# Kernel optimization log

Hardware: AMD Instinct MI355X
Metric: run time of the kernel (lower is better)

## Reference

```python
import jax, jax.numpy as jnp
import numpy as np

TOP_K = 2  # config.moe_config['moe_top_k']


def setup_inputs() -> dict:
    key = jax.random.key(0)
    k1, k2, k3, k4 = jax.random.split(key, 4)
    B, S, H, F, E = 2, 1024, 1024, 2048, 8
    def init(k, shape, fan_in):
        return jax.random.normal(k, shape, jnp.float32) / np.float32(np.sqrt(fan_in))
    return {
        "hidden_states": jax.random.normal(k1, (B, S, H), jnp.float32),
        "router_w": init(k2, (H, E), H),          # Linear(hidden, E, bias=False)
        "W1": init(k3, (E, H, 2 * F), H),          # per-expert Linear(hidden, 2*ffn)
        "W2": init(k4, (E, F, H), F),              # per-expert Linear(ffn, hidden)
    }


def reference(hidden_states, router_w, W1, W2):
    B, S, H = hidden_states.shape
    E = router_w.shape[1]
    x = hidden_states.reshape(-1, H)                      # [N, H], N = B*S
    N = x.shape[0]

    # router: logits -> fp32 softmax -> top-k -> renormalize (matches torch)
    logits = x @ router_w                                  # [N, E]
    probs = jax.nn.softmax(logits.astype(jnp.float32), axis=-1)
    rw, sel = jax.lax.top_k(probs, TOP_K)                  # [N, k]
    rw = rw / rw.sum(axis=-1, keepdims=True)
    rw = rw.astype(x.dtype)

    # combine weights per (token, expert); top-k experts are distinct so add==set
    cw = jnp.zeros((N, E), x.dtype).at[jnp.arange(N)[:, None], sel].add(rw)

    # per-expert SwiGLU MLP over all tokens, masked combine (full-capacity MoE)
    h = jnp.einsum('nh,ehf->enf', x, W1)                   # [E, N, 2F]
    a, b = jnp.split(h, 2, axis=-1)                        # gate, value halves
    g = jax.nn.silu(a) * b                                 # [E, N, F]
    y = jnp.einsum('enf,efh->enh', g, W2)                  # [E, N, H]
    out = jnp.einsum('enh,ne->nh', y, cw)                  # weighted scatter-combine
    return out.reshape(B, S, H)
```

## Files before the change

kernel.cpp:

```cpp
#include <hip/hip_runtime.h>
#include <hip/hip_bf16.h>

#define H_DIM 1024
#define E_NUM 8
#define F_DIM 2048
#define N_TOK 2048
typedef unsigned int uint;
typedef short bf16x8 __attribute__((ext_vector_type(8)));
typedef float f32x4 __attribute__((ext_vector_type(4)));

#define WS_CNT   0
#define WS_OFF   64
#define WS_LIST  256
#define WS_W     (WS_LIST + 8*N_TOK*4)
#define WS_G     131072
#define WS_AX    (WS_G + 4096*2048*2)
#define WS_Y     WS_AX


static __device__ __forceinline__ uint f2bf(float f) {
    uint u = __builtin_bit_cast(uint, f);
    return (u + 0x7FFFu + ((u >> 16) & 1u)) >> 16;
}
static __device__ __forceinline__ float bflo(uint u) { return __builtin_bit_cast(float, u << 16); }
static __device__ __forceinline__ float bfhi(uint u) { return __builtin_bit_cast(float, u & 0xFFFF0000u); }
static __device__ __forceinline__ uint cvtpk(float a, float b) {
    uint r;
    asm("v_cvt_pk_bf16_f32 %0, %1, %2" : "=v"(r) : "v"(a), "v"(b));
    return r;
}
static __device__ __forceinline__ void gload_lds16(const void* g, void* l) {
    __builtin_amdgcn_global_load_lds(
        (const __attribute__((address_space(1))) unsigned int*)g,
        (__attribute__((address_space(3))) unsigned int*)l,
        16, 0, 0);
}
template<int N> static __device__ __forceinline__ void vmwait() {
    if constexpr (N == 0)      asm volatile("s_waitcnt vmcnt(0)" ::: "memory");
    else if constexpr (N == 2) asm volatile("s_waitcnt vmcnt(2)" ::: "memory");
    else if constexpr (N == 4) asm volatile("s_waitcnt vmcnt(4)" ::: "memory");
}
static __device__ __forceinline__ void lgk0_bar() {
    asm volatile("s_waitcnt lgkmcnt(0)" ::: "memory");
    __builtin_amdgcn_sched_barrier(0);
    __builtin_amdgcn_s_barrier();
    asm volatile("" ::: "memory");
}

__global__ __launch_bounds__(256) void router_kernel(
    const float* __restrict__ x, const float* __restrict__ rw,
    int* __restrict__ cnt, int* __restrict__ list, float* __restrict__ w_entry)
{
    int wave = threadIdx.x >> 6, lane = threadIdx.x & 63;
    int n = blockIdx.x * 4 + wave;
    const float* xr = x + (size_t)n * H_DIM;
    float acc[8] = {0,0,0,0,0,0,0,0};
    #pragma unroll
    for (int i = 0; i < H_DIM/64; ++i) {
        int h = i*64 + lane;
        float xv = xr[h];
        const float4* rr = (const float4*)(rw + (size_t)h*8);
        float4 r0 = rr[0], r1 = rr[1];
        acc[0] += xv*r0.x; acc[1] += xv*r0.y; acc[2] += xv*r0.z; acc[3] += xv*r0.w;
        acc[4] += xv*r1.x; acc[5] += xv*r1.y; acc[6] += xv*r1.z; acc[7] += xv*r1.w;
    }
    #pragma unroll
    for (int e = 0; e < 8; ++e) {
        float v = acc[e];
        #pragma unroll
        for (int off = 32; off; off >>= 1) v += __shfl_xor(v, off);
        acc[e] = v;
    }
    int e0 = 0;
    #pragma unroll
    for (int e = 1; e < 8; ++e) if (acc[e] > acc[e0]) e0 = e;
    int e1 = -1;
    #pragma unroll
    for (int e = 0; e < 8; ++e) if (e != e0 && (e1 < 0 || acc[e] > acc[e1])) e1 = e;
    float w0 = 1.0f / (1.0f + __expf(acc[e1] - acc[e0]));
    float w1 = 1.0f - w0;
    if (lane == 0) {
        int p0 = atomicAdd(&cnt[e0], 1);
        list[e0*N_TOK + p0] = n*2;
        w_entry[n*2] = w0;
        int p1 = atomicAdd(&cnt[e1], 1);
        list[e1*N_TOK + p1] = n*2 + 1;
        w_entry[n*2+1] = w1;
    }
}

__global__ void prefix_kernel(const int* __restrict__ cnt, int* __restrict__ off) {
    if (threadIdx.x == 0) {
        int s = 0;
        #pragma unroll
        for (int e = 0; e < E_NUM; ++e) { off[e] = s; s += cnt[e]; }
        off[E_NUM] = s;
    }
}

__global__ __launch_bounds__(256) void gather_kernel(
    const float* __restrict__ x, const int* __restrict__ cnt, const int* __restrict__ off,
    const int* __restrict__ list, unsigned short* __restrict__ Ax)
{
    int e = blockIdx.x >> 9;
    int r = (blockIdx.x & 511)*4 + (threadIdx.x >> 6);
    int lane = threadIdx.x & 63;
    if (r >= cnt[e]) return;
    int ent = list[e*N_TOK + r];
    const float* xr = x + (size_t)(ent >> 1) * H_DIM;
    unsigned short* dr = Ax + (size_t)(off[e] + r) * H_DIM;
    #pragma unroll
    for (int q = 0; q < 2; ++q) {
        int b = lane*2 + q;
        int t = b >> 3, s = b & 7;
        int klo = t*64 + (s >> 2)*32 + (s & 3)*4;
        float4 lo = *(const float4*)(xr + klo);
        float4 hi = *(const float4*)(xr + klo + 16);
        uint4 o;
        o.x = cvtpk(lo.x, lo.y); o.y = cvtpk(lo.z, lo.w);
        o.z = cvtpk(hi.x, hi.y); o.w = cvtpk(hi.z, hi.w);
        *(uint4*)(dr + b*8) = o;
    }
}

template<int IS_G1>
__global__ __launch_bounds__(256, IS_G1 ? 3 : 5) void moe_gemm_kernel(
    const unsigned short* __restrict__ Asrc, const float* __restrict__ W,
    const int* __restrict__ cnt, const int* __restrict__ off,
    const int* __restrict__ list, const float* __restrict__ w_entry,
    unsigned short* __restrict__ dst)
{
    constexpr int KTOT  = IS_G1 ? H_DIM : F_DIM;
    constexpr int BLD   = IS_G1 ? 2*F_DIM : H_DIM;
    constexpr int DLD   = IS_G1 ? F_DIM : H_DIM;
    constexpr int ALD   = IS_G1 ? H_DIM : F_DIM;
    constexpr int ROWS  = IS_G1 ? 128 : 64;
    constexpr int NM    = IS_G1 ? 8 : 2;
    constexpr int NA    = IS_G1 ? 4 : 2;
    constexpr int NMT   = IS_G1 ? 16 : 32;
    constexpr int NNT   = IS_G1 ? 32 : 16;
    constexpr int BSROW = IS_G1 ? 512 : 256;
    constexpr int NBS   = IS_G1 ? 2 : 1;
    constexpr int NT2   = KTOT / 64;

    __shared__ __align__(16) unsigned short As[2][ROWS*64];
    __shared__ __align__(16) uint Bs[2][16*BSROW/4];

    constexpr int nb = NMT * NNT * E_NUM;
    constexpr int chunk = nb >> 3;
    int bid = blockIdx.x;
    int f  = (bid & 7) * chunk + (bid >> 3);
    int mt = f % NMT;
    int nt = (f / NMT) % NNT;
    int e  = f / (NMT * NNT);

    const int c = cnt[e];
    if (mt * ROWS >= c) return;
    const int abase = off[e] + mt * ROWS;
    const int tid = threadIdx.x;
    const int lane = tid & 63, wid = tid >> 6;
    const int l15 = lane & 15, lg = lane >> 4;
    const int wr = IS_G1 ? 0 : (wid >> 1);
    const int wc = wid & 1;
    const int rowbase = IS_G1 ? 0 : wr*32;

    const unsigned short* a_src[NA];
    #pragma unroll
    for (int i = 0; i < NA; ++i) {
        int sl  = wid*(NA*1024) + i*1024 + lane*16;
        int row = sl >> 7;
        int kb  = ((sl >> 4) & 7) ^ (row & 7);
        int gr  = abase + row; gr = gr < 4095 ? gr : 4095;
        a_src[i] = Asrc + (size_t)gr * ALD + kb*8;
    }

    const float* Wb = W + (size_t)e * (size_t)(IS_G1 ? H_DIM*2*F_DIM : F_DIM*H_DIM);
    const float* b_src[NBS]; int b_dst[NBS];
    #pragma unroll
    for (int s = 0; s < NBS; ++s) {
        int q = tid + s*256;
        int kp, c4, gc;
        if constexpr (IS_G1) {
            kp = q >> 5; c4 = q & 31;
            gc = (c4 < 16) ? (nt*64 + 4*c4) : (F_DIM + nt*64 + 4*(c4-16));
        } else {
            kp = q >> 4; c4 = q & 15;
            gc = nt*64 + 4*c4;
        }
        b_src[s] = Wb + (size_t)(2*kp) * BLD + gc;
        b_dst[s] = (kp*BSROW + c4*16) ^ ((kp & 4) << 4);
    }

    int a_addr[NM][2];
    #pragma unroll
    for (int m = 0; m < NM; ++m)
        #pragma unroll
        for (int p = 0; p < 2; ++p) {
            int row = rowbase + m*16 + l15;
            a_addr[m][p] = row*128 + ((p*64 + lg*16) ^ ((row & 7) << 4));
        }
    int b_base[2];
    const int xorv = ((2*lg) & 4) << 4;
    #pragma unroll
    for (int j = 0; j < 2; ++j) {
        int cb = IS_G1 ? (j ? (4 + wid) : wid) : (wc*2 + j);
        b_base[j] = (2*lg)*BSROW + (((cb*16 + l15) * 4) ^ xorv);
    }

    f32x4 acc[NM][2];
    #pragma unroll
    for (int m = 0; m < NM; ++m)
        #pragma unroll
        for (int j = 0; j < 2; ++j) acc[m][j] = (f32x4){0.f,0.f,0.f,0.f};

    struct BQ { float4 r0[NBS], r1[NBS]; };
    auto loadB = [&](int t) {
        BQ q;
        #pragma unroll
        for (int s = 0; s < NBS; ++s) {
            const float* p = b_src[s] + (size_t)t * 32 * BLD;
            q.r0[s] = *(const float4*)p;
            q.r1[s] = *(const float4*)(p + BLD);
        }
        return q;
    };
    auto dswB = [&](const BQ& q, int buf) {
        #pragma unroll
        for (int s = 0; s < NBS; ++s) {
            uint4 w4;
            w4.x = cvtpk(q.r0[s].x, q.r1[s].x); w4.y = cvtpk(q.r0[s].y, q.r1[s].y);
            w4.z = cvtpk(q.r0[s].z, q.r1[s].z); w4.w = cvtpk(q.r0[s].w, q.r1[s].w);
            *(uint4*)((char*)Bs[buf] + b_dst[s]) = w4;
        }
    };
    auto STAGE_A = [&](int a) {
        #pragma unroll
        for (int i = 0; i < NA; ++i)
            gload_lds16(a_src[i] + a*64, (char*)As[a & 1] + wid*(NA*1024) + i*1024);
    };
    auto compute = [&](int P, int abuf) {
        const char* ab  = (const char*)As[abuf];
        const char* bb0 = (const char*)Bs[P];
        bf16x8 bfr[2];
        #pragma unroll
        for (int j = 0; j < 2; ++j) {
            const char* bb = bb0 + b_base[j];
            union { uint u[4]; bf16x8 v; } bu;
            bu.u[0] = *(const uint*)(bb);
            bu.u[1] = *(const uint*)(bb + BSROW);
            bu.u[2] = *(const uint*)(bb + 8*BSROW);
            bu.u[3] = *(const uint*)(bb + 9*BSROW);
            bfr[j] = bu.v;
        }
        #pragma unroll
        for (int m = 0; m < NM; ++m) {
            bf16x8 af = *(const bf16x8*)(ab + (P ? a_addr[m][1] : a_addr[m][0]));
            #pragma unroll
            for (int j = 0; j < 2; ++j)
                acc[m][j] = __builtin_amdgcn_mfma_f32_16x16x32_bf16(af, bfr[j], acc[m][j], 0, 0, 0);
        }
    };

    STAGE_A(0);
    { BQ q0 = loadB(0); dswB(q0, 0); }
    BQ qW = loadB(1);
    BQ qN;

    for (int tp = 0; tp < NT2 - 1; ++tp) {
        vmwait<2*NBS>(); __builtin_amdgcn_sched_barrier(0);
        lgk0_bar();
        STAGE_A(tp + 1);
        qN = loadB(2*tp + 2);
        compute(0, tp & 1);
        dswB(qW, 1);
        lgk0_bar();
        qW = loadB(2*tp + 3);
        compute(1, tp & 1);
        dswB(qN, 0);
    }
    {
        const int ab = (NT2 - 1) & 1;
        vmwait<2*NBS>(); __builtin_amdgcn_sched_barrier(0);
        lgk0_bar();
        compute(0, ab);
        dswB(qW, 1);
        lgk0_bar();
        compute(1, ab);
    }

    if constexpr (IS_G1) {
        const int pbase = nt*64 + ((wid >> 1)*4 + (l15 >> 2))*8 + (wid & 1)*4 + (l15 & 3);
        #pragma unroll
        for (int m = 0; m < NM; ++m) {
            f32x4 ga = acc[m][0], gv = acc[m][1];
            #pragma unroll
            for (int i = 0; i < 4; ++i) {
                int rl = m*16 + lg*4 + i;
                if (mt*ROWS + rl < c) {
                    float a = ga[i];
                    float g = (a / (1.f + __expf(-a))) * gv[i];
                    dst[(size_t)(abase + rl) * DLD + pbase] = (unsigned short)f2bf(g);
                }
            }
        }
    } else {
        const int lbase = e * N_TOK + mt * ROWS;
        #pragma unroll
        for (int m = 0; m < NM; ++m)
            #pragma unroll
            for (int i = 0; i < 4; ++i) {
                int rl = rowbase + m*16 + lg*4 + i;
                if (mt*ROWS + rl < c) {
                    int ent = list[lbase + rl];
                    float w = w_entry[ent];
                    #pragma unroll
                    for (int j = 0; j < 2; ++j) {
                        int col = nt*64 + wc*32 + j*16 + l15;
                        dst[(size_t)ent * DLD + col] = (unsigned short)f2bf(w * acc[m][j][i]);
                    }
                }
            }
    }
}

__global__ __launch_bounds__(256) void combine_kernel(
    const unsigned short* __restrict__ y, float* __restrict__ out)
{
    int gid = blockIdx.x * 256 + threadIdx.x;
    size_t base = (size_t)gid * 8;
    int n = (int)(base >> 10), h = (int)(base & 1023);
    const uint4 a = *(const uint4*)(y + (size_t)(2*n)   * 1024 + h);
    const uint4 b = *(const uint4*)(y + (size_t)(2*n+1) * 1024 + h);
    float4 o0, o1;
    o0.x = bflo(a.x)+bflo(b.x); o0.y = bfhi(a.x)+bfhi(b.x);
    o0.z = bflo(a.y)+bflo(b.y); o0.w = bfhi(a.y)+bfhi(b.y);
    o1.x = bflo(a.z)+bflo(b.z); o1.y = bfhi(a.z)+bfhi(b.z);
    o1.z = bflo(a.w)+bflo(b.w); o1.w = bfhi(a.w)+bfhi(b.w);
    *(float4*)(out + base)     = o0;
    *(float4*)(out + base + 4) = o1;
}

extern "C" void kernel_launch(void* const* d_in, const int* in_sizes, int n_in,
                              void* d_out, int out_size, void* d_ws, size_t ws_size,
                              hipStream_t stream) {
    const float* x  = (const float*)d_in[0];
    const float* rw = (const float*)d_in[1];
    const float* W1 = (const float*)d_in[2];
    const float* W2 = (const float*)d_in[3];
    float* out = (float*)d_out;
    char* ws = (char*)d_ws;
    int*   cnt     = (int*)(ws + WS_CNT);
    int*   off     = (int*)(ws + WS_OFF);
    int*   list    = (int*)(ws + WS_LIST);
    float* w_entry = (float*)(ws + WS_W);
    unsigned short* g  = (unsigned short*)(ws + WS_G);
    unsigned short* Ax = (unsigned short*)(ws + WS_AX);
    unsigned short* y  = (unsigned short*)(ws + WS_Y);

    hipMemsetAsync(cnt, 0, E_NUM * sizeof(int), stream);
    router_kernel<<<N_TOK/4, 256, 0, stream>>>(x, rw, cnt, list, w_entry);
    prefix_kernel<<<1, 64, 0, stream>>>(cnt, off);
    gather_kernel<<<E_NUM*512, 256, 0, stream>>>(x, cnt, off, list, Ax);
    moe_gemm_kernel<1><<<16*32*E_NUM, 256, 0, stream>>>(Ax, W1, cnt, off, list, w_entry, g);
    moe_gemm_kernel<0><<<32*16*E_NUM, 256, 0, stream>>>(g,  W2, cnt, off, list, w_entry, y);
    combine_kernel<<<(out_size/8 + 255)/256, 256, 0, stream>>>(y, out);
}
```

Measured before the change: 204.8 us.

## Pre-convert expert weights to swizzled bf16 tiles before MoE GEMMs

Adds per-call kernels that convert fp32 W1/W2 into bf16 tiles laid out and XOR-swizzled for direct LDS loading. New GEMM kernels stream these packed tiles with global_load_lds, avoiding repeated fp32 weight reads and in-kernel conversion across M tiles. This costs an extra full pass over the weights every call and a large workspace requirement. It falls back to the old kernels if the workspace is too small.

```diff
diff --git a/kernel.cpp b/kernel.cpp
--- a/kernel.cpp
+++ b/kernel.cpp
@@ -16,6 +16,9 @@
 #define WS_G     131072
 #define WS_AX    (WS_G + 4096*2048*2)
 #define WS_Y     WS_AX
+#define WS_W1P   25296896ull
+#define WS_W2P   (WS_W1P + 67108864ull)
+#define WS_NEED  (WS_W2P + 33554432ull)
 
 
 static __device__ __forceinline__ uint f2bf(float f) {
@@ -37,11 +40,19 @@
 }
 template<int N> static __device__ __forceinline__ void vmwait() {
     if constexpr (N == 0)      asm volatile("s_waitcnt vmcnt(0)" ::: "memory");
+    else if constexpr (N == 1) asm volatile("s_waitcnt vmcnt(1)" ::: "memory");
     else if constexpr (N == 2) asm volatile("s_waitcnt vmcnt(2)" ::: "memory");
+    else if constexpr (N == 3) asm volatile("s_waitcnt vmcnt(3)" ::: "memory");
     else if constexpr (N == 4) asm volatile("s_waitcnt vmcnt(4)" ::: "memory");
+    else if constexpr (N == 6) asm volatile("s_waitcnt vmcnt(6)" ::: "memory");
 }
 static __device__ __forceinline__ void lgk0_bar() {
     asm volatile("s_waitcnt lgkmcnt(0)" ::: "memory");
+    __builtin_amdgcn_sched_barrier(0);
+    __builtin_amdgcn_s_barrier();
+    asm volatile("" ::: "memory");
+}
+static __device__ __forceinline__ void raw_bar() {
     __builtin_amdgcn_sched_barrier(0);
     __builtin_amdgcn_s_barrier();
     asm volatile("" ::: "memory");
@@ -120,6 +131,215 @@
         o.x = cvtpk(lo.x, lo.y); o.y = cvtpk(lo.z, lo.w);
         o.z = cvtpk(hi.x, hi.y); o.w = cvtpk(hi.z, hi.w);
         *(uint4*)(dr + b*8) = o;
+    }
+}
+
+template<int IS_G1>
+__global__ __launch_bounds__(256) void prep_w_kernel(
+    const float* __restrict__ W, unsigned short* __restrict__ Wp)
+{
+    constexpr int NNT   = IS_G1 ? 32 : 16;
+    constexpr int NSTEP = IS_G1 ? 32 : 64;
+    constexpr int BLD   = IS_G1 ? 2*F_DIM : H_DIM;
+    constexpr int BSROW = IS_G1 ? 512 : 256;
+    constexpr int TILEB = 16 * BSROW;
+    constexpr int NGR   = TILEB / 16;
+    constexpr int C4N   = IS_G1 ? 32 : 16;
+
+    int bid = blockIdx.x;
+    int t  = bid % NSTEP;
+    int nt = (bid / NSTEP) % NNT;
+    int e  = bid / (NSTEP * NNT);
+    const float* Wb = W + (size_t)e * (size_t)(IS_G1 ? H_DIM*2*F_DIM : F_DIM*H_DIM);
+    char* tile = (char*)Wp + (size_t)bid * TILEB;
+
+    #pragma unroll
+    for (int s = 0; s < NGR/256; ++s) {
+        int gidx = threadIdx.x + s*256;
+        int kp = gidx / C4N, c4 = gidx % C4N;
+        int k  = t*32 + 2*kp;
+        int gc;
+        if constexpr (IS_G1) gc = (c4 < 16) ? (nt*64 + 4*c4) : (F_DIM + nt*64 + 4*(c4-16));
+        else                 gc = nt*64 + 4*c4;
+        const float* p = Wb + (size_t)k * BLD + gc;
+        float4 r0 = *(const float4*)p;
+        float4 r1 = *(const float4*)(p + BLD);
+        uint4 w4;
+        w4.x = cvtpk(r0.x, r1.x); w4.y = cvtpk(r0.y, r1.y);
+        w4.z = cvtpk(r0.z, r1.z); w4.w = cvtpk(r0.w, r1.w);
+        *(uint4*)(tile + ((kp*BSROW + c4*16) ^ ((kp & 4) << 4))) = w4;
+    }
+}
+
+template<int IS_G1>
+__global__ __launch_bounds__(256, IS_G1 ? 3 : 5) void moe_gemm_pre(
+    const unsigned short* __restrict__ Asrc, const unsigned short* __restrict__ Wp,
+    const int* __restrict__ cnt, const int* __restrict__ off,
+    const int* __restrict__ list, const float* __restrict__ w_entry,
+    unsigned short* __restrict__ dst)
+{
+    constexpr int KTOT  = IS_G1 ? H_DIM : F_DIM;
+    constexpr int DLD   = IS_G1 ? F_DIM : H_DIM;
+    constexpr int ALD   = IS_G1 ? H_DIM : F_DIM;
+    constexpr int ROWS  = IS_G1 ? 128 : 64;
+    constexpr int NM    = IS_G1 ? 8 : 2;
+    constexpr int NA    = IS_G1 ? 4 : 2;
+    constexpr int NMT   = IS_G1 ? 16 : 32;
+    constexpr int NNT   = IS_G1 ? 32 : 16;
+    constexpr int BSROW = IS_G1 ? 512 : 256;
+    constexpr int TILEB = 16 * BSROW;
+    constexpr int NBSG  = TILEB / 4096;
+    constexpr int NSTEP = KTOT / 32;
+    constexpr int NP    = KTOT / 64;
+
+    __shared__ __align__(16) unsigned short As[2][ROWS*64];
+    __shared__ __align__(16) uint Bs[2][TILEB/4];
+
+    constexpr int nb = NMT * NNT * E_NUM;
+    constexpr int chunk = nb >> 3;
+    int bid = blockIdx.x;
+    int f  = (bid & 7) * chunk + (bid >> 3);
+    int mt = f % NMT;
+    int nt = (f / NMT) % NNT;
+    int e  = f / (NMT * NNT);
+
+    const int c = cnt[e];
+    if (mt * ROWS >= c) return;
+    const int abase = off[e] + mt * ROWS;
+    const int tid = threadIdx.x;
+    const int lane = tid & 63, wid = tid >> 6;
+    const int l15 = lane & 15, lg = lane >> 4;
+    const int wr = IS_G1 ? 0 : (wid >> 1);
+    const int wc = wid & 1;
+    const int rowbase = IS_G1 ? 0 : wr*32;
+
+    const unsigned short* a_src[NA];
+    #pragma unroll
+    for (int i = 0; i < NA; ++i) {
+        int sl  = wid*(NA*1024) + i*1024 + lane*16;
+        int row = sl >> 7;
+        int kb  = ((sl >> 4) & 7) ^ (row & 7);
+        int gr  = abase + row; gr = gr < 4095 ? gr : 4095;
+        a_src[i] = Asrc + (size_t)gr * ALD + kb*8;
+    }
+    const unsigned short* bp = Wp + (size_t)((e*NNT + nt)*NSTEP) * (TILEB/2)
+                             + wid*(TILEB/8) + lane*8;
+
+    int a_addr[NM][2];
+    #pragma unroll
+    for (int m = 0; m < NM; ++m)
+        #pragma unroll
+        for (int p = 0; p < 2; ++p) {
+            int row = rowbase + m*16 + l15;
+            a_addr[m][p] = row*128 + ((p*64 + lg*16) ^ ((row & 7) << 4));
+        }
+    int b_base[2];
+    const int xorv = ((2*lg) & 4) << 4;
+    #pragma unroll
+    for (int j = 0; j < 2; ++j) {
+        int cb = IS_G1 ? (j ? (4 + wid) : wid) : (wc*2 + j);
+        b_base[j] = (2*lg)*BSROW + (((cb*16 + l15) * 4) ^ xorv);
+    }
+
+    f32x4 acc[NM][2];
+    #pragma unroll
+    for (int m = 0; m < NM; ++m)
+        #pragma unroll
+        for (int j = 0; j < 2; ++j) acc[m][j] = (f32x4){0.f,0.f,0.f,0.f};
+
+    auto STAGE_A = [&](int p) {
+        #pragma unroll
+        for (int i = 0; i < NA; ++i)
+            gload_lds16(a_src[i] + p*64, (char*)As[p & 1] + wid*(NA*1024) + i*1024);
+    };
+    auto STAGE_B = [&](int t) {
+        #pragma unroll
+        for (int i = 0; i < NBSG; ++i)
+            gload_lds16(bp + (size_t)t*(TILEB/2) + i*512,
+                        (char*)Bs[t & 1] + wid*(TILEB/4) + i*1024);
+    };
+    auto compute = [&](int P, int abuf) {
+        const char* ab  = (const char*)As[abuf];
+        const char* bb0 = (const char*)Bs[P];
+        bf16x8 bfr[2];
+        #pragma unroll
+        for (int j = 0; j < 2; ++j) {
+            const char* bb = bb0 + b_base[j];
+            union { uint u[4]; bf16x8 v; } bu;
+            bu.u[0] = *(const uint*)(bb);
+            bu.u[1] = *(const uint*)(bb + BSROW);
+            bu.u[2] = *(const uint*)(bb + 8*BSROW);
+            bu.u[3] = *(const uint*)(bb + 9*BSROW);
+            bfr[j] = bu.v;
+        }
+        #pragma unroll
+        for (int m = 0; m < NM; ++m) {
+            bf16x8 af = *(const bf16x8*)(ab + (P ? a_addr[m][1] : a_addr[m][0]));
+            #pragma unroll
+            for (int j = 0; j < 2; ++j)
+                acc[m][j] = __builtin_amdgcn_mfma_f32_16x16x32_bf16(af, bfr[j], acc[m][j], 0, 0, 0);
+        }
+    };
+
+    STAGE_A(0);
+    STAGE_B(0);
+    STAGE_B(1);
+
+    for (int p = 0; p < NP - 1; ++p) {
+        vmwait<NBSG>();
+        raw_bar();
+        compute(0, p & 1);
+        raw_bar();
+        STAGE_B(2*p + 2);
+        STAGE_A(p + 1);
+        vmwait<NBSG + NA>();
+        raw_bar();
+        compute(1, p & 1);
+        raw_bar();
+        STAGE_B(2*p + 3);
+    }
+    {
+        const int ab = (NP - 1) & 1;
+        vmwait<NBSG>();
+        raw_bar();
+        compute(0, ab);
+        vmwait<0>();
+        raw_bar();
+        compute(1, ab);
+    }
+
+    if constexpr (IS_G1) {
+        const int pbase = nt*64 + ((wid >> 1)*4 + (l15 >> 2))*8 + (wid & 1)*4 + (l15 & 3);
+        #pragma unroll
+        for (int m = 0; m < NM; ++m) {
+            f32x4 ga = acc[m][0], gv = acc[m][1];
+            #pragma unroll
+            for (int i = 0; i < 4; ++i) {
+                int rl = m*16 + lg*4 + i;
+                if (mt*ROWS + rl < c) {
+                    float a = ga[i];
+                    float g = (a / (1.f + __expf(-a))) * gv[i];
+                    dst[(size_t)(abase + rl) * DLD + pbase] = (unsigned short)f2bf(g);
+                }
+            }
+        }
+    } else {
+        const int lbase = e * N_TOK + mt * ROWS;
+        #pragma unroll
+        for (int m = 0; m < NM; ++m)
+            #pragma unroll
+            for (int i = 0; i < 4; ++i) {
+                int rl = rowbase + m*16 + lg*4 + i;
+                if (mt*ROWS + rl < c) {
+                    int ent = list[lbase + rl];
+                    float w = w_entry[ent];
+                    #pragma unroll
+                    for (int j = 0; j < 2; ++j) {
+                        int col = nt*64 + wc*32 + j*16 + l15;
+                        dst[(size_t)ent * DLD + col] = (unsigned short)f2bf(w * acc[m][j][i]);
+                    }
+                }
+            }
     }
 }
 
@@ -361,7 +581,17 @@
     router_kernel<<<N_TOK/4, 256, 0, stream>>>(x, rw, cnt, list, w_entry);
     prefix_kernel<<<1, 64, 0, stream>>>(cnt, off);
     gather_kernel<<<E_NUM*512, 256, 0, stream>>>(x, cnt, off, list, Ax);
-    moe_gemm_kernel<1><<<16*32*E_NUM, 256, 0, stream>>>(Ax, W1, cnt, off, list, w_entry, g);
-    moe_gemm_kernel<0><<<32*16*E_NUM, 256, 0, stream>>>(g,  W2, cnt, off, list, w_entry, y);
+
+    if (ws_size >= WS_NEED) {
+        unsigned short* W1p = (unsigned short*)(ws + WS_W1P);
+        unsigned short* W2p = (unsigned short*)(ws + WS_W2P);
+        prep_w_kernel<1><<<E_NUM*32*32, 256, 0, stream>>>(W1, W1p);
+        prep_w_kernel<0><<<E_NUM*16*64, 256, 0, stream>>>(W2, W2p);
+        moe_gemm_pre<1><<<16*32*E_NUM, 256, 0, stream>>>(Ax, W1p, cnt, off, list, w_entry, g);
+        moe_gemm_pre<0><<<32*16*E_NUM, 256, 0, stream>>>(g,  W2p, cnt, off, list, w_entry, y);
+    } else {
+        moe_gemm_kernel<1><<<16*32*E_NUM, 256, 0, stream>>>(Ax, W1, cnt, off, list, w_entry, g);
+        moe_gemm_kernel<0><<<32*16*E_NUM, 256, 0, stream>>>(g,  W2, cnt, off, list, w_entry, y);
+    }
     combine_kernel<<<(out_size/8 + 255)/256, 256, 0, stream>>>(y, out);
 }
```

New measurement: 242.0 us. 1.18x slower.
